# Optimization experiments

Measured on AMD Instinct MI355X. Metric: run time of the kernel, lower is better.

Reference implementation:

```python
import jax, jax.numpy as jnp
import numpy as np

B, N, NE = 16, 96, 256
ATOM, EDIM, HID, LAT, HEADS = 128, 16, 128, 128, 4
HD = LAT // HEADS
RBF, CUT, ZEMB, MAXZ = 16, 5.0, 32, 100
MUL0_IN, MUL1_IN = 64, 32      # irreps_node = 64x0e + 32x1o (dim 160)
MUL0_OUT, MUL1_OUT = 32, 16    # out irreps  = 32x0e + 16x1o (dim 80)
NODE_DIM = MUL0_IN + 3 * MUL1_IN
OUT_DIM = MUL0_OUT + 3 * MUL1_OUT
E_ATT = 1024
WNUM = MUL0_IN*MUL0_OUT + MUL0_IN*MUL1_OUT + MUL1_IN*MUL1_OUT + MUL1_IN*MUL0_OUT  # 4608


def _mlp3(x, w1, b1, w2, b2, w3, b3):
    x = jax.nn.silu(x @ w1 + b1)
    x = jax.nn.silu(x @ w2 + b2)
    return x @ w3 + b3


def setup_inputs() -> dict:
    key = jax.random.key(0)
    ks = jax.random.split(key, 40)
    s = 0.05  # scale params so deep MLP activations stay numerically sane
    d = {}
    d['h'] = jax.random.normal(ks[0], (B, N, ATOM), jnp.float32)
    d['h_full'] = jax.random.normal(ks[1], (B, N, NODE_DIM), jnp.float32)
    d['e_feat'] = jax.random.normal(ks[2], (NE, EDIM), jnp.float32)
    d['att_dist'] = jax.random.uniform(ks[3], (E_ATT,), jnp.float32)
    d['att_vec'] = jax.random.normal(ks[4], (E_ATT, 3), jnp.float32)
    d['z_emb_table'] = jax.random.normal(ks[5], (MAXZ + 1, ZEMB), jnp.float32) * s
    d['rw1'] = jax.random.normal(ks[6], (ZEMB + 1 + RBF, HID), jnp.float32) * s
    d['rb1'] = jnp.zeros((HID,), jnp.float32)
    d['rw2'] = jax.random.normal(ks[7], (HID, WNUM), jnp.float32) * s
    d['rb2'] = jnp.zeros((WNUM,), jnp.float32)
    d['ew1'] = jax.random.normal(ks[8], (EDIM, HID), jnp.float32) * s
    d['eb1'] = jnp.zeros((HID,), jnp.float32)
    d['ew2'] = jax.random.normal(ks[9], (HID, MUL0_OUT + MUL1_OUT), jnp.float32) * s
    d['eb2'] = jnp.zeros((MUL0_OUT + MUL1_OUT,), jnp.float32)
    d['qw1'] = jax.random.normal(ks[10], (ATOM + EDIM, HID), jnp.float32) * s
    d['qb1'] = jnp.zeros((HID,), jnp.float32)
    d['qw2'] = jax.random.normal(ks[11], (HID, HID), jnp.float32) * s
    d['qb2'] = jnp.zeros((HID,), jnp.float32)
    d['qw3'] = jax.random.normal(ks[12], (HID, LAT), jnp.float32) * s
    d['qb3'] = jnp.zeros((LAT,), jnp.float32)
    d['kw1'] = jax.random.normal(ks[13], (ATOM + ZEMB + 1 + RBF, HID), jnp.float32) * s
    d['kb1'] = jnp.zeros((HID,), jnp.float32)
    d['kw2'] = jax.random.normal(ks[14], (HID, HID), jnp.float32) * s
    d['kb2'] = jnp.zeros((HID,), jnp.float32)
    d['kw3'] = jax.random.normal(ks[15], (HID, LAT), jnp.float32) * s
    d['kb3'] = jnp.zeros((LAT,), jnp.float32)
    d['ow1'] = jax.random.normal(ks[16], (MUL0_OUT + MUL1_OUT, HID), jnp.float32) * s
    d['ob1'] = jnp.zeros((HID,), jnp.float32)
    d['ow2'] = jax.random.normal(ks[17], (HID, HID), jnp.float32) * s
    d['ob2'] = jnp.zeros((HID,), jnp.float32)
    d['ow3'] = jax.random.normal(ks[18], (HID, LAT), jnp.float32) * s
    d['ob3'] = jnp.zeros((LAT,), jnp.float32)
    d['z'] = jax.random.randint(ks[19], (B, N), 0, MAXZ)
    d['mask'] = jnp.ones((B, N), bool)
    d['absorber_index'] = jax.random.randint(ks[20], (B,), 0, N)
    d['att_dst'] = jnp.arange(E_ATT)  # unique flat indices into B*N
    return d


def reference(h, h_full, e_feat, att_dist, att_vec, z_emb_table,
              rw1, rb1, rw2, rb2, ew1, eb1, ew2, eb2,
              qw1, qb1, qw2, qb2, qw3, qb3,
              kw1, kb1, kw2, kb2, kw3, kb3,
              ow1, ob1, ow2, ob2, ow3, ob3,
              z, mask, absorber_index, att_dst):
    Bz, Na, Hd = h.shape
    F = Bz * Na
    nE = e_feat.shape[0]
    # scatter edge data into flat (B*N) atom slots
    am_flat = jnp.zeros((F,), bool).at[att_dst].set(True)
    d_flat = jnp.zeros((F,), h.dtype).at[att_dst].set(att_dist)
    v_flat = jnp.zeros((F, 3), h.dtype).at[att_dst].set(att_vec)
    att_mask = am_flat.reshape(Bz, Na) & mask
    # spherical harmonics (lmax=1, component normalization): Y0 = 1, Y1 = sqrt(3)*unit_vec
    un = v_flat / jnp.maximum(jnp.linalg.norm(v_flat, axis=-1, keepdims=True), 1e-8)
    y1 = jnp.sqrt(3.0) * un
    # Gaussian RBF on absorber->atom distance
    mu = jnp.linspace(0.0, CUT, RBF)
    delta = CUT / (RBF - 1)
    rbf = jnp.exp(-(d_flat[:, None] - mu) ** 2 / (2.0 * delta * delta))  # (F, RBF)
    zr = z_emb_table[z]                      # (B, N, ZEMB)
    zr_flat = zr.reshape(F, -1)
    is_abs = jnp.zeros((Bz, Na), h.dtype).at[jnp.arange(Bz), absorber_index].set(1.0)
    # radial MLP -> per-edge tensor-product weights
    w_in = jnp.concatenate([zr_flat, is_abs.reshape(F, 1), rbf], -1)
    tpw = jax.nn.silu(w_in @ rw1 + rb1) @ rw2 + rb2  # (F, WNUM)
    s1 = MUL0_IN * MUL0_OUT
    s2 = s1 + MUL0_IN * MUL1_OUT
    s3 = s2 + MUL1_IN * MUL1_OUT
    w00 = tpw[:, :s1].reshape(F, MUL0_IN, MUL0_OUT)   # 0e x 0e -> 0e
    w01 = tpw[:, s1:s2].reshape(F, MUL0_IN, MUL1_OUT) # 0e x 1o -> 1o
    w10 = tpw[:, s2:s3].reshape(F, MUL1_IN, MUL1_OUT) # 1o x 0e -> 1o
    w11 = tpw[:, s3:].reshape(F, MUL1_IN, MUL0_OUT)   # 1o x 1o -> 0e
    hf = h_full.reshape(F, -1)
    x0 = hf[:, :MUL0_IN]
    x1 = hf[:, MUL0_IN:].reshape(F, MUL1_IN, 3)
    alpha = 1.0 / jnp.sqrt(jnp.float32(MUL0_IN + MUL1_IN))  # path fan-in normalization
    c = 1.0 / jnp.sqrt(3.0)                                  # wigner-3j coeff for l=1 couplings
    out0 = alpha * (jnp.einsum('fi,fio->fo', x0, w00)
                    + c * jnp.einsum('fim,fm,fio->fo', x1, y1, w11))
    out1 = alpha * c * (jnp.einsum('fi,fm,fio->fom', x0, y1, w01)
                        + jnp.einsum('fim,fio->fom', x1, w10))
    v_irrep = jnp.concatenate([out0, out1.reshape(F, 3 * MUL1_OUT)], -1)  # (F, OUT_DIM)
    # cosine cutoff envelope + edge mask
    env = jnp.where(d_flat < CUT, 0.5 * (jnp.cos(jnp.pi * d_flat / CUT) + 1.0), 0.0)
    v_irrep = v_irrep * (am_flat.astype(h.dtype) * env)[:, None]
    # energy-conditioned per-irrep-channel modulation
    gates = jax.nn.silu(e_feat @ ew1 + eb1) @ ew2 + eb2  # (nE, 48)
    g_exp = jnp.concatenate([gates[:, :MUL0_OUT],
                             jnp.repeat(gates[:, MUL0_OUT:], 3, axis=-1)], -1)  # (nE, OUT_DIM)
    v_mod = (v_irrep[:, None, :] * g_exp[None]).reshape(Bz, Na, nE, OUT_DIM)
    # invariant multi-head scoring
    h_abs = h[jnp.arange(Bz), absorber_index]  # (B, H)
    q_in = jnp.concatenate([jnp.broadcast_to(h_abs[:, None], (Bz, nE, Hd)),
                            jnp.broadcast_to(e_feat[None], (Bz, nE, EDIM))], -1)
    q = _mlp3(q_in, qw1, qb1, qw2, qb2, qw3, qb3)  # (B, nE, LAT)
    atom_static = jnp.concatenate([h, zr, is_abs[..., None], rbf.reshape(Bz, Na, RBF)], -1)
    k = _mlp3(atom_static, kw1, kb1, kw2, kb2, kw3, kb3)  # (B, N, LAT)
    qh = q.reshape(Bz, nE, HEADS, HD)
    kh = k.reshape(Bz, Na, HEADS, HD)
    scores = (jnp.einsum('behd,bnhd->benh', qh, kh) * (HD ** -0.5)).mean(-1)  # (B, nE, N)
    m = att_mask[:, None, :]
    scores = jnp.where(m, scores, -1e9)
    attn = jax.nn.softmax(scores, axis=2) * m.astype(h.dtype)
    attn = attn / jnp.maximum(attn.sum(2, keepdims=True), 1e-8)
    out_irrep = jnp.einsum('ben,bnec->bec', attn, v_mod)  # (B, nE, OUT_DIM)
    # invariants: scalars + vector norms
    scal = out_irrep[..., :MUL0_OUT]
    vec = out_irrep[..., MUL0_OUT:].reshape(Bz, nE, MUL1_OUT, 3)
    inv = jnp.concatenate([scal, jnp.sqrt(jnp.sum(vec * vec, -1) + 1e-12)], -1)
    return _mlp3(inv, ow1, ob1, ow2, ob2, ow3, ob3)  # (B, nE, LAT)
```

## Files before the change

### kernel.cpp

```cpp
#include <hip/hip_runtime.h>
#include <hip/hip_fp16.h>
#include <math.h>

#define BB 16
#define NN 96
#define NE 256
#define FF (BB*NN)
#define ATOM 128
#define EDIM 16
#define HID 128
#define LAT 128
#define RBFN 16
#define CUTOFF 5.0f
#define ZEMB 32
#define E_ATT 1024
#define M0I 64
#define M1I 32
#define M0O 32
#define M1O 16
#define NODE_DIM 160
#define OUT_DIM 80
#define INVD 48
#define WNUM 4608

#define K1_TP 192
#define K1_EDGE_AT 192
#define K1_Q_AT 448
#define K1_GATE_AT 960
#define K1_PREP_AT 976
#define K1_BLKS 977

typedef _Float16 half8_t __attribute__((ext_vector_type(8)));
typedef float float4v __attribute__((ext_vector_type(4)));

__device__ __forceinline__ float silu_f(float x) { return x / (1.0f + expf(-x)); }

__global__ __launch_bounds__(256) void k1(
    const float* __restrict__ h, const float* __restrict__ h_full,
    const float* __restrict__ z_emb, const int* __restrict__ z,
    const int* __restrict__ absorber, const float* __restrict__ e_feat,
    const int* __restrict__ att_dst, const float* __restrict__ att_dist,
    const float* __restrict__ att_vec,
    const float* __restrict__ rw1, const float* __restrict__ rb1,
    const float* __restrict__ rw2, const float* __restrict__ rb2,
    const float* __restrict__ kw1, const float* __restrict__ kb1,
    const float* __restrict__ kw2, const float* __restrict__ kb2,
    const float* __restrict__ kw3, const float* __restrict__ kb3,
    const float* __restrict__ qw1, const float* __restrict__ qb1,
    const float* __restrict__ qw2, const float* __restrict__ qb2,
    const float* __restrict__ qw3, const float* __restrict__ qb3,
    const float* __restrict__ ew1, const float* __restrict__ eb1,
    const float* __restrict__ ew2, const float* __restrict__ eb2,
    float* __restrict__ kmatw, float* __restrict__ qmat,
    float* __restrict__ gexp, float* __restrict__ virr,
    int* __restrict__ inv)
{
    __shared__ __align__(16) char smemraw[38592];
    float* smem = (float*)smemraw;
    int blk = blockIdx.x;
    int t = threadIdx.x;

    if (blk < K1_TP) {
        __half* cS    = (__half*)smemraw;
        float*  winf  = (float*)smemraw;
        float*  fbase = (float*)(smemraw + 4352);
        float* x0f  = fbase;
        float* x1f  = fbase + 1024;
        float* xyf  = fbase + 2560;
        float* y1f  = fbase + 3072;
        float* envf = fbase + 3136;
        float* dS   = fbase + 3152;
        int*   fI   = (int*)(fbase + 3168);
        _Float16* hS = (_Float16*)(smemraw + 17088);
        __half*   Bs = (__half*)(smemraw + 21184);

        int cls  = blk % 3;
        int tile16 = blk / 3;
        int e0t = tile16 * 16;
        int clsAdd = (cls == 1) ? 1 : 0;
        if (t < 16) {
            int e = e0t + t;
            int f = att_dst[e];
            fI[t] = f;
            float d = att_dist[e];
            dS[t] = d;
            envf[t] = (d < CUTOFF) ? 0.5f*(cosf(3.14159265358979323846f*d/CUTOFF) + 1.0f) : 0.0f;
            float vx = att_vec[3*e], vy = att_vec[3*e+1], vz = att_vec[3*e+2];
            float nrm = sqrtf(vx*vx + vy*vy + vz*vz);
            float is = 1.0f / fmaxf(nrm, 1e-8f);
            const float s3 = 1.7320508075688772f;
            y1f[t*4]   = s3*vx*is;
            y1f[t*4+1] = s3*vy*is;
            y1f[t*4+2] = s3*vz*is;
        }
        __syncthreads();
        for (int u = t; u < 16*49; u += 256) {
            int e = u / 49, j = u - 49*(u/49);
            int f = fI[e];
            float v;
            if (j < ZEMB) v = z_emb[z[f]*ZEMB + j];
            else if (j == ZEMB) { int b = f / NN, nn = f - b*NN; v = (absorber[b] == nn) ? 1.0f : 0.0f; }
            else {
                int jr = j - 33;
                const float delta = CUTOFF / (RBFN - 1);
                float diff = dS[e] - jr*delta;
                v = expf(-diff*diff / (2.0f*delta*delta));
            }
            winf[e*52 + j] = v;
        }
        for (int p = 0; p < 10; p++) {
            int idx = t + 256*p;
            int edge = idx / 160, j = idx - 160*edge;
            float v = h_full[fI[edge]*NODE_DIM + j];
            if (j < M0I) x0f[edge*64 + j] = v;
            else         x1f[edge*96 + (j - M0I)] = v;
        }
        __syncthreads();
        for (int p = 0; p < 2; p++) {
            int idx = t + 256*p;
            int edge = idx >> 5, i = idx & 31;
            xyf[edge*32 + i] = x1f[edge*96 + 3*i]*y1f[edge*4]
                             + x1f[edge*96 + 3*i+1]*y1f[edge*4+1]
                             + x1f[edge*96 + 3*i+2]*y1f[edge*4+2];
        }
        {
            int e = t >> 4;
            const float* wf = winf + e*52;
            #pragma unroll
            for (int p = 0; p < 4; p++) {
                int c2 = 2*((t & 15) + 16*p);
                float2 a0 = *(const float2*)&rb1[c2];
                float2 a1 = make_float2(0.f, 0.f);
                #pragma unroll 8
                for (int i = 0; i < 48; i += 2) {
                    float x0v = wf[i], x1v = wf[i + 1];
                    float2 w0 = *(const float2*)&rw1[i*HID + c2];
                    float2 w1 = *(const float2*)&rw1[(i+1)*HID + c2];
                    a0.x += x0v*w0.x; a0.y += x0v*w0.y;
                    a1.x += x1v*w1.x; a1.y += x1v*w1.y;
                }
                {
                    float x0v = wf[48];
                    float2 w0 = *(const float2*)&rw1[48*HID + c2];
                    a0.x += x0v*w0.x; a0.y += x0v*w0.y;
                }
                *(__half2*)&hS[e*128 + c2] =
                    __floats2half2_rn(silu_f(a0.x + a1.x), silu_f(a0.y + a1.y));
            }
        }
        {
            int kk = (t >> 2) & 63;
            int n4 = t & 3;
            #pragma unroll
            for (int p = 0; p < 4; p++) {
                int j = 0*4 + p;
                int ntg = (cls == 2) ? (128 + j) : (2*j + clsAdd + ((j >= 64) ? 96 : 0));
                const float* src = rw2 + (2*kk)*WNUM + ntg*16 + n4*4;
                float4 va = *(const float4*)src;
                float4 vb = *(const float4*)(src + WNUM);
                __half* bp = Bs + p*2176 + (n4*4)*136 + 2*kk;
                *(__half2*)(bp)         = __floats2half2_rn(va.x, vb.x);
                *(__half2*)(bp + 136)   = __floats2half2_rn(va.y, vb.y);
                *(__half2*)(bp + 272)   = __floats2half2_rn(va.z, vb.z);
                *(__half2*)(bp + 408)   = __floats2half2_rn(va.w, vb.w);
            }
        }
        __syncthreads();

        int wv = t >> 6;
        int lane = t & 63;
        int mrow = lane & 15, quad = lane >> 4;
        half8_t af[4];
        #pragma unroll
        for (int kc = 0; kc < 4; kc++)
            af[kc] = *(const half8_t*)&hS[mrow*128 + quad*8 + kc*32];

        int edge = t >> 4, o = t & 15;
        int kkS = (t >> 2) & 63;
        int n4S = t & 3;
        float t00 = 0.f, t11 = 0.f;
        float t01 = 0.f, tm0 = 0.f, tm1 = 0.f, tm2 = 0.f;

        for (int g = 0; g < 24; g++) {
            {
                int j = g*4 + wv;
                int ntg = (cls == 2) ? (128 + j) : (2*j + clsAdd + ((j >= 64) ? 96 : 0));
                float4v acc = {0.f, 0.f, 0.f, 0.f};
                #pragma unroll
                for (int kc = 0; kc < 4; kc++) {
                    half8_t bfr = *(const half8_t*)&((_Float16*)Bs)[wv*2176 + mrow*136 + kc*32 + quad*8];
                    acc = __builtin_amdgcn_mfma_f32_16x16x32_f16(af[kc], bfr, acc, 0, 0, 0);
                }
                float bias = rb2[ntg*16 + mrow];
                #pragma unroll
                for (int r = 0; r < 4; r++)
                    cS[(quad*4 + r)*136 + wv*16 + mrow] = __float2half(acc[r] + bias);
            }
            __syncthreads();
            if (g + 1 < 24) {
                #pragma unroll
                for (int p = 0; p < 4; p++) {
                    int j = (g+1)*4 + p;
                    int ntg = (cls == 2) ? (128 + j) : (2*j + clsAdd + ((j >= 64) ? 96 : 0));
                    const float* src = rw2 + (2*kkS)*WNUM + ntg*16 + n4S*4;
                    float4 va = *(const float4*)src;
                    float4 vb = *(const float4*)(src + WNUM);
                    __half* bp = Bs + p*2176 + (n4S*4)*136 + 2*kkS;
                    *(__half2*)(bp)       = __floats2half2_rn(va.x, vb.x);
                    *(__half2*)(bp + 136) = __floats2half2_rn(va.y, vb.y);
                    *(__half2*)(bp + 272) = __floats2half2_rn(va.z, vb.z);
                    *(__half2*)(bp + 408) = __floats2half2_rn(va.w, vb.w);
                }
            }
            {
                const __half* cRow = cS + edge*136 + o;
                if (cls < 2) {
                    if (g < 16) {
                        #pragma unroll
                        for (int nt = 0; nt < 4; nt++)
                            t00 += x0f[edge*64 + g*4 + nt]*__half2float(cRow[nt*16]);
                    } else {
                        #pragma unroll
                        for (int nt = 0; nt < 4; nt++)
                            t11 += xyf[edge*32 + (g*4 + nt - 64)]*__half2float(cRow[nt*16]);
                    }
                } else {
                    if (g < 16) {
                        #pragma unroll
                        for (int nt = 0; nt < 4; nt++)
                            t01 += x0f[edge*64 + g*4 + nt]*__half2float(cRow[nt*16]);
                    } else {
                        #pragma unroll
                        for (int nt = 0; nt < 4; nt++) {
                            int i = g*4 + nt - 64;
                            float C = __half2float(cRow[nt*16]);
                            tm0 += x1f[edge*96 + 3*i]*C;
                            tm1 += x1f[edge*96 + 3*i+1]*C;
                            tm2 += x1f[edge*96 + 3*i+2]*C;
                        }
                    }
                }
            }
            __syncthreads();
        }
        const float alpha = 0.10206207261596575f;
        const float ccf   = 0.5773502691896258f;
        int f = fI[edge];
        float env = envf[edge];
        if (cls < 2) {
            virr[f*OUT_DIM + cls*16 + o] = alpha*(t00 + ccf*t11)*env;
        } else {
            float y0 = y1f[edge*4], y1v = y1f[edge*4+1], y2 = y1f[edge*4+2];
            virr[f*OUT_DIM + M0O + 3*o]     = alpha*ccf*(t01*y0 + tm0)*env;
            virr[f*OUT_DIM + M0O + 3*o + 1] = alpha*ccf*(t01*y1v + tm1)*env;
            virr[f*OUT_DIM + M0O + 3*o + 2] = alpha*ccf*(t01*y2 + tm2)*env;
        }
    } else if (blk < K1_Q_AT) {
        float (*sin1)[184] = (float(*)[184])smem;
        float (*l1S)[128]  = (float(*)[128])(smem + 736);
        float (*l2S)[128]  = (float(*)[128])(smem + 736 + 512);
        int w = t >> 6;
        int c = t & 63;
        int e = (blk - K1_EDGE_AT)*4 + w;
        int f = att_dst[e];
        int b = f / NN, nn = f - b*NN;
        float d = att_dist[e];
        {
            float2 hv = *(const float2*)&h[f*ATOM + 2*c];
            sin1[w][2*c] = hv.x; sin1[w][2*c + 1] = hv.y;
        }
        if (c < ZEMB) sin1[w][ATOM + c] = z_emb[z[f]*ZEMB + c];
        if (c >= 32 && c < 48) {
            int j = c - 32;
            const float delta = CUTOFF / (RBFN - 1);
            float diff = d - j*delta;
            sin1[w][ATOM + ZEMB + 1 + j] = expf(-diff*diff / (2.0f*delta*delta));
        }
        if (c == 48) sin1[w][ATOM + ZEMB] = (absorber[b] == nn) ? 1.0f : 0.0f;
        __syncthreads();
        int c2 = 2*c;
        {
            float2 a0 = *(const float2*)&kb1[c2];
            float2 a1 = make_float2(0.f, 0.f);
            #pragma unroll 8
            for (int i = 0; i < 176; i += 2) {
                float x0v = sin1[w][i], x1v = sin1[w][i + 1];
                float2 w0 = *(const float2*)&kw1[i*HID + c2];
                float2 w1 = *(const float2*)&kw1[(i+1)*HID + c2];
                a0.x += x0v*w0.x; a0.y += x0v*w0.y;
                a1.x += x1v*w1.x; a1.y += x1v*w1.y;
            }
            {
                float x0v = sin1[w][176];
                float2 w0 = *(const float2*)&kw1[176*HID + c2];
                a0.x += x0v*w0.x; a0.y += x0v*w0.y;
            }
            l1S[w][c2] = silu_f(a0.x + a1.x); l1S[w][c2+1] = silu_f(a0.y + a1.y);
        }
        __syncthreads();
        {
            float2 a0 = *(const float2*)&kb2[c2];
            float2 a1 = make_float2(0.f, 0.f);
            #pragma unroll 8
            for (int i = 0; i < HID; i += 2) {
                float x0v = l1S[w][i], x1v = l1S[w][i + 1];
                float2 w0 = *(const float2*)&kw2[i*HID + c2];
                float2 w1 = *(const float2*)&kw2[(i+1)*HID + c2];
                a0.x += x0v*w0.x; a0.y += x0v*w0.y;
                a1.x += x1v*w1.x; a1.y += x1v*w1.y;
            }
            l2S[w][c2] = silu_f(a0.x + a1.x); l2S[w][c2+1] = silu_f(a0.y + a1.y);
        }
        __syncthreads();
        {
            float2 a0 = *(const float2*)&kb3[c2];
            float2 a1 = make_float2(0.f, 0.f);
            #pragma unroll 8
            for (int i = 0; i < HID; i += 2) {
                float x0v = l2S[w][i], x1v = l2S[w][i + 1];
                float2 w0 = *(const float2*)&kw3[i*HID + c2];
                float2 w1 = *(const float2*)&kw3[(i+1)*HID + c2];
                a0.x += x0v*w0.x; a0.y += x0v*w0.y;
                a1.x += x1v*w1.x; a1.y += x1v*w1.y;
            }
            float2 o; o.x = a0.x + a1.x; o.y = a0.y + a1.y;
            *(float2*)&kmatw[f*HID + c2] = o;
        }
    } else if (blk < K1_GATE_AT) {
        float* hA          = smem;
        float (*ef)[16]    = (float(*)[16])(smem + 128);
        float (*part)[128] = (float(*)[128])(smem + 256);
        float* l1S         = smem + 1280;
        float* l2S         = smem + 2304;
        int idx = blk - K1_Q_AT;
        int r0 = idx * 8;
        int b  = r0 >> 8;
        int e8 = r0 & 255;
        if (t < 32) *(float4*)&hA[t*4] = *(const float4*)&h[(b*NN + absorber[b])*ATOM + t*4];
        if (t >= 128 && t < 256) { int e = (t - 128) >> 4, j = t & 15; ef[e][j] = e_feat[(e8 + e)*EDIM + j]; }
        __syncthreads();
        int r = t >> 5, c0 = (t & 31)*4;
        {
            float4 a0 = make_float4(0,0,0,0);
            int k0 = r*16;
            #pragma unroll
            for (int k = 0; k < 16; k++) {
                float hv = hA[k0 + k];
                float4 w0 = *(const float4*)&qw1[(k0 + k)*HID + c0];
                a0.x += hv*w0.x; a0.y += hv*w0.y; a0.z += hv*w0.z; a0.w += hv*w0.w;
            }
            *(float4*)&part[r][c0] = a0;
        }
        __syncthreads();
        {
            float4 s = *(const float4*)&qb1[c0];
            #pragma unroll
            for (int g = 0; g < 8; g++) {
                float4 pg = *(const float4*)&part[g][c0];
                s.x += pg.x; s.y += pg.y; s.z += pg.z; s.w += pg.w;
            }
            #pragma unroll
            for (int j = 0; j < 16; j++) {
                float a = ef[r][j];
                float4 w0 = *(const float4*)&qw1[(ATOM + j)*HID + c0];
                s.x += a*w0.x; s.y += a*w0.y; s.z += a*w0.z; s.w += a*w0.w;
            }
            l1S[r*128 + c0]   = silu_f(s.x); l1S[r*128 + c0+1] = silu_f(s.y);
            l1S[r*128 + c0+2] = silu_f(s.z); l1S[r*128 + c0+3] = silu_f(s.w);
        }
        __syncthreads();
        {
            float4 a0 = *(const float4*)&qb2[c0];
            float4 a1 = make_float4(0,0,0,0);
            #pragma unroll 8
            for (int i = 0; i < HID; i += 2) {
                float x0v = l1S[r*128 + i], x1v = l1S[r*128 + i+1];
                float4 w0 = *(const float4*)&qw2[i*HID + c0];
                float4 w1 = *(const float4*)&qw2[(i+1)*HID + c0];
                a0.x += x0v*w0.x; a0.y += x0v*w0.y; a0.z += x0v*w0.z; a0.w += x0v*w0.w;
                a1.x += x1v*w1.x; a1.y += x1v*w1.y; a1.z += x1v*w1.z; a1.w += x1v*w1.w;
            }
            l2S[r*128 + c0]   = silu_f(a0.x + a1.x); l2S[r*128 + c0+1] = silu_f(a0.y + a1.y);
            l2S[r*128 + c0+2] = silu_f(a0.z + a1.z); l2S[r*128 + c0+3] = silu_f(a0.w + a1.w);
        }
        __syncthreads();
        {
            float4 a0 = *(const float4*)&qb3[c0];
            float4 a1 = make_float4(0,0,0,0);
            #pragma unroll 8
            for (int i = 0; i < HID; i += 2) {
                float x0v = l2S[r*128 + i], x1v = l2S[r*128 + i+1];
                float4 w0 = *(const float4*)&qw3[i*HID + c0];
                float4 w1 = *(const float4*)&qw3[(i+1)*HID + c0];
                a0.x += x0v*w0.x; a0.y += x0v*w0.y; a0.z += x0v*w0.z; a0.w += x0v*w0.w;
                a1.x += x1v*w1.x; a1.y += x1v*w1.y; a1.z += x1v*w1.z; a1.w += x1v*w1.w;
            }
            float4 o;
            o.x = a0.x + a1.x; o.y = a0.y + a1.y; o.z = a0.z + a1.z; o.w = a0.w + a1.w;
            *(float4*)&qmat[(r0 + r)*LAT + c0] = o;
        }
    } else if (blk < K1_PREP_AT) {
        float (*ef)[16]   = (float(*)[16])smem;
        float (*l1g)[128] = (float(*)[128])(smem + 256);
        float (*gg)[48]   = (float(*)[48])(smem + 256 + 2048);
        int e0 = (blk - K1_GATE_AT) * 16;
        { int e = t >> 4, i = t & 15; ef[e][i] = e_feat[(e0 + e)*EDIM + i]; }
        __syncthreads();
        int r = t >> 4, c0 = (t & 15)*8;
        {
            float4 a0 = *(const float4*)&eb1[c0];
            float4 a1 = *(const float4*)&eb1[c0 + 4];
            #pragma unroll
            for (int i = 0; i < EDIM; i++) {
                float a = ef[r][i];
                float4 w0 = *(const float4*)&ew1[i*HID + c0];
                float4 w1 = *(const float4*)&ew1[i*HID + c0 + 4];
                a0.x += a*w0.x; a0.y += a*w0.y; a0.z += a*w0.z; a0.w += a*w0.w;
                a1.x += a*w1.x; a1.y += a*w1.y; a1.z += a*w1.z; a1.w += a*w1.w;
            }
            l1g[r][c0]   = silu_f(a0.x); l1g[r][c0+1] = silu_f(a0.y);
            l1g[r][c0+2] = silu_f(a0.z); l1g[r][c0+3] = silu_f(a0.w);
            l1g[r][c0+4] = silu_f(a1.x); l1g[r][c0+5] = silu_f(a1.y);
            l1g[r][c0+6] = silu_f(a1.z); l1g[r][c0+7] = silu_f(a1.w);
        }
        __syncthreads();
        for (int u = t; u < 16*48; u += 256) {
            int e = u / 48, j = u - 48*(u/48);
            float acc = eb2[j];
            #pragma unroll 4
            for (int i = 0; i < HID; i++) acc += l1g[e][i]*ew2[i*48 + j];
            gg[e][j] = acc;
        }
        __syncthreads();
        for (int u = t; u < 16*80; u += 256) {
            int e = u / 80, cc = u - 80*(u/80);
            gexp[(e0 + e)*OUT_DIM + cc] = (cc < M0O) ? gg[e][cc] : gg[e][M0O + (cc - M0O)/3];
        }
    } else {
        for (int p = 0; p < 6; p++) inv[t + 256*p] = -1;
        __syncthreads();
        for (int p = 0; p < 4; p++) { int e = t + 256*p; inv[att_dst[e]] = e; }
    }
}

__global__ __launch_bounds__(256) void k_attf(
    const float* __restrict__ qmat, const float* __restrict__ kmat,
    const int* __restrict__ inv,
    const float* __restrict__ virr, const float* __restrict__ gexp,
    const float* __restrict__ ow1, const float* __restrict__ ob1,
    const float* __restrict__ ow2, const float* __restrict__ ob2,
    const float* __restrict__ ow3, const float* __restrict__ ob3,
    float* __restrict__ out)
{
    int u0 = blockIdx.x;
    int b  = u0 >> 6;
    int e0 = (u0 & 63) * 4;
    int t = threadIdx.x;
    __shared__ float smem[6816];
    float* aS  = smem;
    float* gS  = smem + 400;
    float* pvS = smem + 736;
    float* ocS = smem + 1408;
    float* mS  = smem + 1744;
    float* inS = smem + 1840;
    float* q4  = smem + 2032;
    float* Kt  = smem + 2560;
    float* l1S = smem + 2560;
    float* l2S = smem + 3072;

    if (t < 80) {
        int el = t / 20, c4 = t - 20*(t/20);
        *(float4*)&gS[el*84 + c4*4] = *(const float4*)&gexp[(e0 + el)*OUT_DIM + c4*4];
    }
    if (t < NN) mS[t] = ((unsigned)inv[b*NN + t] < E_ATT) ? 1.0f : 0.0f;
    int row = t >> 6, ln = t & 63;
    *(float2*)&q4[row*132 + ln*2] = *(const float2*)&qmat[(b*NE + e0 + row)*LAT + ln*2];

    float sacc_a = 0.f, sacc_b = 0.f;
    #pragma unroll
    for (int nt = 0; nt < 3; nt++) {
        __syncthreads();
        for (int p = 0; p < 4; p++) {
            int idx = t + 256*p; int n = idx >> 5, i4 = idx & 31;
            *(float4*)&Kt[n*133 + i4*4] = *(const float4*)&kmat[(b*NN + nt*32 + n)*LAT + i4*4];
        }
        __syncthreads();
        if ((ln >> 5) == nt) {
            const float* kp = &Kt[(ln & 31)*133];
            const float* qp = &q4[row*132];
            float a0 = 0.f, a1 = 0.f;
            #pragma unroll 16
            for (int i = 0; i < LAT; i += 2) {
                a0 += qp[i]*kp[i];
                a1 += qp[i+1]*kp[i+1];
            }
            sacc_a = a0 + a1;
        }
        if (nt == 2 && ln < 32) {
            const float* kp = &Kt[ln*133];
            const float* qp = &q4[row*132];
            float a0 = 0.f, a1 = 0.f;
            #pragma unroll 16
            for (int i = 0; i < LAT; i += 2) {
                a0 += qp[i]*kp[i];
                a1 += qp[i+1]*kp[i+1];
            }
            sacc_b = a0 + a1;
        }
    }

    {
        const float scale = 0.04419417382415922f;
        float m_a = mS[ln];
        float m_b = (ln < 32) ? mS[64 + ln] : 0.f;
        float s_a = (m_a != 0.f) ? sacc_a*scale : -1e9f;
        float s_b = (m_b != 0.f) ? sacc_b*scale : -1e9f;
        float mx = fmaxf(s_a, s_b);
        #pragma unroll
        for (int off = 1; off < 64; off <<= 1) mx = fmaxf(mx, __shfl_xor(mx, off));
        float e_a = expf(s_a - mx), e_b = expf(s_b - mx);
        float sm = e_a + e_b;
        #pragma unroll
        for (int off = 1; off < 64; off <<= 1) sm += __shfl_xor(sm, off);
        float r = 1.0f / sm;
        float p_a = m_a*e_a*r, p_b = m_b*e_b*r;
        float ss = p_a + p_b;
        #pragma unroll
        for (int off = 1; off < 64; off <<= 1) ss += __shfl_xor(ss, off);
        float is = 1.0f / fmaxf(ss, 1e-8f);
        aS[row*100 + ln] = p_a*is;
        if (ln < 32) aS[row*100 + 64 + ln] = p_b*is;
    }
    __syncthreads();

    if (t < 160) {
        int prow = t / 40, idx = t % 40;
        int half = idx / 20, c4 = idx % 20;
        const float* vp = virr + (long)b*NN*OUT_DIM + c4*4;
        float4 acc = make_float4(0,0,0,0);
        int n0 = half*48;
        #pragma unroll 8
        for (int n = n0; n < n0 + 48; n++) {
            float a = aS[prow*100 + n];
            float4 v = *(const float4*)&vp[n*OUT_DIM];
            acc.x += a*v.x; acc.y += a*v.y; acc.z += a*v.z; acc.w += a*v.w;
        }
        *(float4*)&pvS[prow*168 + half*84 + c4*4] = acc;
    }
    __syncthreads();
    if (t < 80) {
        int prow = t / 20, c4 = t % 20;
        float4 A = *(float4*)&pvS[prow*168 + c4*4];
        float4 Bv = *(float4*)&pvS[prow*168 + 84 + c4*4];
        float4 g = *(float4*)&gS[prow*84 + c4*4];
        float4 o;
        o.x = (A.x + Bv.x)*g.x; o.y = (A.y + Bv.y)*g.y;
        o.z = (A.z + Bv.z)*g.z; o.w = (A.w + Bv.w)*g.w;
        *(float4*)&ocS[prow*84 + c4*4] = o;
    }
    __syncthreads();

    if (t < 4*INVD) {
        int el = t / INVD, j = t - INVD*(t/INVD);
        float val;
        if (j < M0O) val = ocS[el*84 + j];
        else {
            int o = j - M0O;
            float x = ocS[el*84 + M0O + 3*o], y = ocS[el*84 + M0O + 3*o + 1], zz = ocS[el*84 + M0O + 3*o + 2];
            val = sqrtf(x*x + y*y + zz*zz + 1e-12f);
        }
        inS[el*INVD + j] = val;
    }
    __syncthreads();

    int r = t >> 6, cc = (t & 63)*2;
    {
        float2 a0 = *(const float2*)&ob1[cc];
        float2 a1 = make_float2(0.f, 0.f);
        #pragma unroll 8
        for (int i = 0; i < INVD; i += 2) {
            float x0v = inS[r*INVD + i], x1v = inS[r*INVD + i+1];
            float2 w0 = *(const float2*)&ow1[i*HID + cc];
            float2 w1 = *(const float2*)&ow1[(i+1)*HID + cc];
            a0.x += x0v*w0.x; a0.y += x0v*w0.y;
            a1.x += x1v*w1.x; a1.y += x1v*w1.y;
        }
        l1S[r*128 + cc]   = silu_f(a0.x + a1.x);
        l1S[r*128 + cc+1] = silu_f(a0.y + a1.y);
    }
    __syncthreads();
    {
        float2 a0 = *(const float2*)&ob2[cc];
        float2 a1 = make_float2(0.f, 0.f);
        #pragma unroll 8
        for (int i = 0; i < HID; i += 2) {
            float x0v = l1S[r*128 + i], x1v = l1S[r*128 + i+1];
            float2 w0 = *(const float2*)&ow2[i*HID + cc];
            float2 w1 = *(const float2*)&ow2[(i+1)*HID + cc];
            a0.x += x0v*w0.x; a0.y += x0v*w0.y;
            a1.x += x1v*w1.x; a1.y += x1v*w1.y;
        }
        l2S[r*128 + cc]   = silu_f(a0.x + a1.x);
        l2S[r*128 + cc+1] = silu_f(a0.y + a1.y);
    }
    __syncthreads();
    {
        float2 a0 = *(const float2*)&ob3[cc];
        float2 a1 = make_float2(0.f, 0.f);
        #pragma unroll 8
        for (int i = 0; i < HID; i += 2) {
            float x0v = l2S[r*128 + i], x1v = l2S[r*128 + i+1];
            float2 w0 = *(const float2*)&ow3[i*HID + cc];
            float2 w1 = *(const float2*)&ow3[(i+1)*HID + cc];
            a0.x += x0v*w0.x; a0.y += x0v*w0.y;
            a1.x += x1v*w1.x; a1.y += x1v*w1.y;
        }
        float2 o;
        o.x = a0.x + a1.x; o.y = a0.y + a1.y;
        *(float2*)&out[((b*NE + e0) + r)*LAT + cc] = o;
    }
}

extern "C" void kernel_launch(void* const* d_in, const int* in_sizes, int n_in,
                              void* d_out, int out_size, void* d_ws, size_t ws_size,
                              hipStream_t stream) {
    const float* h        = (const float*)d_in[0];
    const float* h_full   = (const float*)d_in[1];
    const float* e_feat   = (const float*)d_in[2];
    const float* att_dist = (const float*)d_in[3];
    const float* att_vec  = (const float*)d_in[4];
    const float* z_emb    = (const float*)d_in[5];
    const float* rw1 = (const float*)d_in[6];  const float* rb1 = (const float*)d_in[7];
    const float* rw2 = (const float*)d_in[8];  const float* rb2 = (const float*)d_in[9];
    const float* ew1 = (const float*)d_in[10]; const float* eb1 = (const float*)d_in[11];
    const float* ew2 = (const float*)d_in[12]; const float* eb2 = (const float*)d_in[13];
    const float* qw1 = (const float*)d_in[14]; const float* qb1 = (const float*)d_in[15];
    const float* qw2 = (const float*)d_in[16]; const float* qb2 = (const float*)d_in[17];
    const float* qw3 = (const float*)d_in[18]; const float* qb3 = (const float*)d_in[19];
    const float* kw1 = (const float*)d_in[20]; const float* kb1 = (const float*)d_in[21];
    const float* kw2 = (const float*)d_in[22]; const float* kb2 = (const float*)d_in[23];
    const float* kw3 = (const float*)d_in[24]; const float* kb3 = (const float*)d_in[25];
    const float* ow1 = (const float*)d_in[26]; const float* ob1 = (const float*)d_in[27];
    const float* ow2 = (const float*)d_in[28]; const float* ob2 = (const float*)d_in[29];
    const float* ow3 = (const float*)d_in[30]; const float* ob3 = (const float*)d_in[31];
    const int* z        = (const int*)d_in[32];
    const int* absorber = (const int*)d_in[34];
    const int* att_dst  = (const int*)d_in[35];

    float* ws = (float*)d_ws;
    int*   inv     = (int*)ws;
    float* kmat    = ws + 5632;
    float* qmat    = ws + 202240;
    float* gexp    = ws + 726528;
    float* virr    = ws + 747008;

    float* out = (float*)d_out;

    k1<<<K1_BLKS, 256, 0, stream>>>(h, h_full, z_emb, z, absorber, e_feat,
                                    att_dst, att_dist, att_vec,
                                    rw1, rb1, rw2, rb2,
                                    kw1, kb1, kw2, kb2, kw3, kb3,
                                    qw1, qb1, qw2, qb2, qw3, qb3,
                                    ew1, eb1, ew2, eb2,
                                    kmat, qmat, gexp, virr, inv);
    k_attf<<<BB*64, 256, 0, stream>>>(qmat, kmat, inv, virr, gexp,
                                      ow1, ob1, ow2, ob2, ow3, ob3, out);
}
```

Measured before the change: 246.5 us.

## Remove per-step LDS staging and barriers from tensor-product MFMA loop

Each wave now owns a contiguous 24-tile slice of the radial weight columns and loads B fragments straight from global rw2 into registers. It contracts the MFMA outputs against node features in registers, then reduces partials across waves once through shared memory. This removes the per-iteration shared staging of B and C and the two barriers per step. In exchange it issues strided scalar global loads for B (stride WNUM per element) with no coalescing, which may raise memory latency. Feature arrays are padded to avoid bank conflicts.

```diff
diff --git a/kernel.cpp b/kernel.cpp
--- a/kernel.cpp
+++ b/kernel.cpp
@@ -55,29 +55,27 @@
     float* __restrict__ gexp, float* __restrict__ virr,
     int* __restrict__ inv)
 {
-    __shared__ __align__(16) char smemraw[38592];
+    __shared__ __align__(16) char smemraw[37760];
     float* smem = (float*)smemraw;
     int blk = blockIdx.x;
     int t = threadIdx.x;
 
     if (blk < K1_TP) {
-        __half* cS    = (__half*)smemraw;
         float*  winf  = (float*)smemraw;
-        float*  fbase = (float*)(smemraw + 4352);
+        float*  fbase = (float*)smemraw + 1088;
         float* x0f  = fbase;
-        float* x1f  = fbase + 1024;
-        float* xyf  = fbase + 2560;
-        float* y1f  = fbase + 3072;
-        float* envf = fbase + 3136;
-        float* dS   = fbase + 3152;
-        int*   fI   = (int*)(fbase + 3168);
-        _Float16* hS = (_Float16*)(smemraw + 17088);
-        __half*   Bs = (__half*)(smemraw + 21184);
+        float* x1f  = fbase + 1040;
+        float* xyf  = fbase + 2592;
+        float* y1f  = fbase + 3120;
+        float* envf = fbase + 3184;
+        float* dS   = fbase + 3200;
+        int*   fI   = (int*)(fbase + 3216);
+        _Float16* hS = (_Float16*)(smemraw + 17280);
+        float* pS   = (float*)(smemraw + 21376);
 
         int cls  = blk % 3;
-        int tile16 = blk / 3;
-        int e0t = tile16 * 16;
-        int clsAdd = (cls == 1) ? 1 : 0;
+        int tile = blk / 3;
+        int e0t = tile * 16;
         if (t < 16) {
             int e = e0t + t;
             int f = att_dst[e];
@@ -112,16 +110,16 @@
             int idx = t + 256*p;
             int edge = idx / 160, j = idx - 160*edge;
             float v = h_full[fI[edge]*NODE_DIM + j];
-            if (j < M0I) x0f[edge*64 + j] = v;
-            else         x1f[edge*96 + (j - M0I)] = v;
+            if (j < M0I) x0f[edge*65 + j] = v;
+            else         x1f[edge*97 + (j - M0I)] = v;
         }
         __syncthreads();
         for (int p = 0; p < 2; p++) {
             int idx = t + 256*p;
             int edge = idx >> 5, i = idx & 31;
-            xyf[edge*32 + i] = x1f[edge*96 + 3*i]*y1f[edge*4]
-                             + x1f[edge*96 + 3*i+1]*y1f[edge*4+1]
-                             + x1f[edge*96 + 3*i+2]*y1f[edge*4+2];
+            xyf[edge*33 + i] = x1f[edge*97 + 3*i]*y1f[edge*4]
+                             + x1f[edge*97 + 3*i+1]*y1f[edge*4+1]
+                             + x1f[edge*97 + 3*i+2]*y1f[edge*4+2];
         }
         {
             int e = t >> 4;
@@ -148,23 +146,6 @@
                     __floats2half2_rn(silu_f(a0.x + a1.x), silu_f(a0.y + a1.y));
             }
         }
-        {
-            int kk = (t >> 2) & 63;
-            int n4 = t & 3;
-            #pragma unroll
-            for (int p = 0; p < 4; p++) {
-                int j = 0*4 + p;
-                int ntg = (cls == 2) ? (128 + j) : (2*j + clsAdd + ((j >= 64) ? 96 : 0));
-                const float* src = rw2 + (2*kk)*WNUM + ntg*16 + n4*4;
-                float4 va = *(const float4*)src;
-                float4 vb = *(const float4*)(src + WNUM);
-                __half* bp = Bs + p*2176 + (n4*4)*136 + 2*kk;
-                *(__half2*)(bp)         = __floats2half2_rn(va.x, vb.x);
-                *(__half2*)(bp + 136)   = __floats2half2_rn(va.y, vb.y);
-                *(__half2*)(bp + 272)   = __floats2half2_rn(va.z, vb.z);
-                *(__half2*)(bp + 408)   = __floats2half2_rn(va.w, vb.w);
-            }
-        }
         __syncthreads();
 
         int wv = t >> 6;
@@ -175,85 +156,86 @@
         for (int kc = 0; kc < 4; kc++)
             af[kc] = *(const half8_t*)&hS[mrow*128 + quad*8 + kc*32];
 
-        int edge = t >> 4, o = t & 15;
-        int kkS = (t >> 2) & 63;
-        int n4S = t & 3;
-        float t00 = 0.f, t11 = 0.f;
-        float t01 = 0.f, tm0 = 0.f, tm1 = 0.f, tm2 = 0.f;
-
-        for (int g = 0; g < 24; g++) {
-            {
-                int j = g*4 + wv;
-                int ntg = (cls == 2) ? (128 + j) : (2*j + clsAdd + ((j >= 64) ? 96 : 0));
-                float4v acc = {0.f, 0.f, 0.f, 0.f};
+        int clsAdd = (cls == 1) ? 1 : 0;
+        float pa[4] = {0.f,0.f,0.f,0.f}, pb[4] = {0.f,0.f,0.f,0.f};
+        float pc[4] = {0.f,0.f,0.f,0.f}, pd[4] = {0.f,0.f,0.f,0.f};
+
+        #pragma unroll 2
+        for (int jj = 0; jj < 24; jj++) {
+            int j = wv*24 + jj;
+            int ntg = (cls == 2) ? (128 + j)
+                                 : (2*j + clsAdd + ((j >= 64) ? 96 : 0));
+            const float* bcol = rw2 + ntg*16 + mrow;
+            float4v acc = {0.f, 0.f, 0.f, 0.f};
+            #pragma unroll
+            for (int kc = 0; kc < 4; kc++) {
+                half8_t bfr;
                 #pragma unroll
-                for (int kc = 0; kc < 4; kc++) {
-                    half8_t bfr = *(const half8_t*)&((_Float16*)Bs)[wv*2176 + mrow*136 + kc*32 + quad*8];
-                    acc = __builtin_amdgcn_mfma_f32_16x16x32_f16(af[kc], bfr, acc, 0, 0, 0);
+                for (int m = 0; m < 8; m++)
+                    bfr[m] = (_Float16)bcol[(quad*8 + kc*32 + m)*WNUM];
+                acc = __builtin_amdgcn_mfma_f32_16x16x32_f16(af[kc], bfr, acc, 0, 0, 0);
+            }
+            float bias = rb2[ntg*16 + mrow];
+            if (cls < 2) {
+                if (j < 64) {
+                    #pragma unroll
+                    for (int r = 0; r < 4; r++)
+                        pa[r] += x0f[(quad*4 + r)*65 + j]*(acc[r] + bias);
+                } else {
+                    #pragma unroll
+                    for (int r = 0; r < 4; r++)
+                        pb[r] += xyf[(quad*4 + r)*33 + (j - 64)]*(acc[r] + bias);
                 }
-                float bias = rb2[ntg*16 + mrow];
-                #pragma unroll
-                for (int r = 0; r < 4; r++)
-                    cS[(quad*4 + r)*136 + wv*16 + mrow] = __float2half(acc[r] + bias);
-            }
-            __syncthreads();
-            if (g + 1 < 24) {
-                #pragma unroll
-                for (int p = 0; p < 4; p++) {
-                    int j = (g+1)*4 + p;
-                    int ntg = (cls == 2) ? (128 + j) : (2*j + clsAdd + ((j >= 64) ? 96 : 0));
-                    const float* src = rw2 + (2*kkS)*WNUM + ntg*16 + n4S*4;
-                    float4 va = *(const float4*)src;
-                    float4 vb = *(const float4*)(src + WNUM);
-                    __half* bp = Bs + p*2176 + (n4S*4)*136 + 2*kkS;
-                    *(__half2*)(bp)       = __floats2half2_rn(va.x, vb.x);
-                    *(__half2*)(bp + 136) = __floats2half2_rn(va.y, vb.y);
-                    *(__half2*)(bp + 272) = __floats2half2_rn(va.z, vb.z);
-                    *(__half2*)(bp + 408) = __floats2half2_rn(va.w, vb.w);
-                }
-            }
-            {
-                const __half* cRow = cS + edge*136 + o;
-                if (cls < 2) {
-                    if (g < 16) {
-                        #pragma unroll
-                        for (int nt = 0; nt < 4; nt++)
-                            t00 += x0f[edge*64 + g*4 + nt]*__half2float(cRow[nt*16]);
-                    } else {
-                        #pragma unroll
-                        for (int nt = 0; nt < 4; nt++)
-                            t11 += xyf[edge*32 + (g*4 + nt - 64)]*__half2float(cRow[nt*16]);
-                    }
+            } else {
+                if (j < 64) {
+                    #pragma unroll
+                    for (int r = 0; r < 4; r++)
+                        pa[r] += x0f[(quad*4 + r)*65 + j]*(acc[r] + bias);
                 } else {
-                    if (g < 16) {
-                        #pragma unroll
-                        for (int nt = 0; nt < 4; nt++)
-                            t01 += x0f[edge*64 + g*4 + nt]*__half2float(cRow[nt*16]);
-                    } else {
-                        #pragma unroll
-                        for (int nt = 0; nt < 4; nt++) {
-                            int i = g*4 + nt - 64;
-                            float C = __half2float(cRow[nt*16]);
-                            tm0 += x1f[edge*96 + 3*i]*C;
-                            tm1 += x1f[edge*96 + 3*i+1]*C;
-                            tm2 += x1f[edge*96 + 3*i+2]*C;
-                        }
+                    int i = j - 64;
+                    #pragma unroll
+                    for (int r = 0; r < 4; r++) {
+                        float C = acc[r] + bias;
+                        pb[r] += x1f[(quad*4 + r)*97 + 3*i]*C;
+                        pc[r] += x1f[(quad*4 + r)*97 + 3*i+1]*C;
+                        pd[r] += x1f[(quad*4 + r)*97 + 3*i+2]*C;
                     }
                 }
             }
-            __syncthreads();
-        }
-        const float alpha = 0.10206207261596575f;
-        const float ccf   = 0.5773502691896258f;
-        int f = fI[edge];
-        float env = envf[edge];
-        if (cls < 2) {
-            virr[f*OUT_DIM + cls*16 + o] = alpha*(t00 + ccf*t11)*env;
-        } else {
-            float y0 = y1f[edge*4], y1v = y1f[edge*4+1], y2 = y1f[edge*4+2];
-            virr[f*OUT_DIM + M0O + 3*o]     = alpha*ccf*(t01*y0 + tm0)*env;
-            virr[f*OUT_DIM + M0O + 3*o + 1] = alpha*ccf*(t01*y1v + tm1)*env;
-            virr[f*OUT_DIM + M0O + 3*o + 2] = alpha*ccf*(t01*y2 + tm2)*env;
+        }
+        #pragma unroll
+        for (int r = 0; r < 4; r++) {
+            int edge = quad*4 + r;
+            pS[((wv*4 + 0)*16 + edge)*16 + mrow] = pa[r];
+            pS[((wv*4 + 1)*16 + edge)*16 + mrow] = pb[r];
+            if (cls == 2) {
+                pS[((wv*4 + 2)*16 + edge)*16 + mrow] = pc[r];
+                pS[((wv*4 + 3)*16 + edge)*16 + mrow] = pd[r];
+            }
+        }
+        __syncthreads();
+        {
+            int edge = t >> 4, o = t & 15;
+            const float alpha = 0.10206207261596575f;
+            const float ccf   = 0.5773502691896258f;
+            int f = fI[edge];
+            float env = envf[edge];
+            float s0 = pS[((0*4+0)*16 + edge)*16 + o] + pS[((1*4+0)*16 + edge)*16 + o]
+                     + pS[((2*4+0)*16 + edge)*16 + o] + pS[((3*4+0)*16 + edge)*16 + o];
+            float s1 = pS[((0*4+1)*16 + edge)*16 + o] + pS[((1*4+1)*16 + edge)*16 + o]
+                     + pS[((2*4+1)*16 + edge)*16 + o] + pS[((3*4+1)*16 + edge)*16 + o];
+            if (cls < 2) {
+                virr[f*OUT_DIM + cls*16 + o] = alpha*(s0 + ccf*s1)*env;
+            } else {
+                float s2 = pS[((0*4+2)*16 + edge)*16 + o] + pS[((1*4+2)*16 + edge)*16 + o]
+                         + pS[((2*4+2)*16 + edge)*16 + o] + pS[((3*4+2)*16 + edge)*16 + o];
+                float s3 = pS[((0*4+3)*16 + edge)*16 + o] + pS[((1*4+3)*16 + edge)*16 + o]
+                         + pS[((2*4+3)*16 + edge)*16 + o] + pS[((3*4+3)*16 + edge)*16 + o];
+                float y0 = y1f[edge*4], y1v = y1f[edge*4+1], y2 = y1f[edge*4+2];
+                virr[f*OUT_DIM + M0O + 3*o]     = alpha*ccf*(s0*y0 + s1)*env;
+                virr[f*OUT_DIM + M0O + 3*o + 1] = alpha*ccf*(s0*y1v + s2)*env;
+                virr[f*OUT_DIM + M0O + 3*o + 2] = alpha*ccf*(s0*y2 + s3)*env;
+            }
         }
     } else if (blk < K1_Q_AT) {
         float (*sin1)[184] = (float(*)[184])smem;
```

Result: faster. 225.1 us (-8.7%).
